# Kernel optimization log

Measured on AMD Instinct MI355X. Metric: run time of the kernel, lower is better.

## Reference

```python
import jax, jax.numpy as jnp
import numpy as np

H, O, M, D, B = 4, 32, 128, 16, 1024
JITTER = 1e-4


def k_rbf(theta, X, Y):
    # theta: [H, 1+D] (log sf2, log lengthscales); X: [O,Mx,D]; Y: [O,My,D]
    sf2 = jnp.exp(theta[:, 0])[:, None, None, None]          # [H,1,1,1]
    ls = jnp.exp(theta[:, 1:])                               # [H,D]
    Xs = X[None] / ls[:, None, None, :]                      # [H,O,Mx,D]
    Ys = Y[None] / ls[:, None, None, :]                      # [H,O,My,D]
    d2 = ((Xs ** 2).sum(-1)[..., :, None]
          + (Ys ** 2).sum(-1)[..., None, :]
          - 2.0 * jnp.einsum('homd,hond->homn', Xs, Ys))
    return sf2 * jnp.exp(-0.5 * jnp.maximum(d2, 0.0))


def vec2tril(vec, m):
    r, c = jnp.tril_indices(m)
    L = jnp.zeros(vec.shape[:-1] + (m, m), vec.dtype)
    return L.at[..., r, c].set(vec)


def _st(Lmat, rhs):
    return jax.scipy.linalg.solve_triangular(Lmat, rhs, lower=True)


def setup_inputs() -> dict:
    key = jax.random.key(0)
    ks = jax.random.split(key, 8)
    eye = jnp.eye(M, dtype=jnp.float32)
    return {
        'x': jax.random.normal(ks[0], (B, D), jnp.float32),
        'z': 0.5 * jax.random.normal(ks[1], (O, M, D), jnp.float32),
        'u_mean': 0.5 * jax.random.normal(ks[2], (O, M, 1), jnp.float32),
        'u_tril_vec': 0.1 * jax.random.normal(ks[3], (O, M * (M + 1) // 2), jnp.float32),
        'm_old': 0.5 * jax.random.normal(ks[4], (O, M, 1), jnp.float32),
        'L_old': jnp.tril(0.1 * jax.random.normal(ks[5], (O, M, M), jnp.float32)) + eye,
        'z_old': 0.5 * jax.random.normal(ks[6], (O, M, D), jnp.float32),
        'theta': 0.1 * jax.random.normal(ks[7], (H, D + 1), jnp.float32),
    }


def reference(x, z, u_mean, u_tril_vec, m_old, L_old, z_old, theta):
    dt = x.dtype
    u_tril = vec2tril(u_tril_vec, M)                          # [O,M,M]
    eyeM = jnp.eye(M, dtype=dt)

    # ---- linear_gauss_joint (one previous task) ----
    kuf = k_rbf(theta, z_old, z)                              # [H,O,M,M]
    kuu = k_rbf(theta, z_old, z_old)                          # [H,O,M,M]
    Lkuu = jnp.linalg.cholesky(kuu + JITTER * eyeM)
    LKinvKuf = _st(Lkuu, kuf)
    m_oldh = jnp.broadcast_to(m_old[None], (H, O, M, 1))
    L_oldh = jnp.broadcast_to(L_old[None], (H, O, M, M))
    LKinvm = _st(Lkuu, m_oldh)
    Am = jnp.einsum('...ij,...ik->...jk', LKinvKuf, LKinvm)   # A @ m_old, [H,O,M,1]
    m_new = Am + u_mean[None]
    m_joint = jnp.concatenate([m_oldh, m_new], axis=-2)       # [H,O,2M,1]

    S_old = jnp.einsum('...ji,...ki->...jk', L_oldh, L_oldh)
    LKinvLS = _st(Lkuu, L_oldh)
    AtX = jnp.einsum('...ij,...ik->...jk', LKinvLS, LKinvKuf)  # [H,O,M,M]
    SoldAt = jnp.einsum('...ji,...ik->...jk', L_oldh, AtX)
    ASoldt = jnp.swapaxes(SoldAt, -1, -2)
    S_cur = jnp.einsum('...ji,...ki->...jk', u_tril, u_tril)[None]
    ASoldAt = jnp.einsum('...ij,...ik->...jk', AtX, AtX)
    cov_joint = jnp.concatenate([
        jnp.concatenate([S_old, SoldAt], axis=-1),
        jnp.concatenate([ASoldt, S_cur + ASoldAt], axis=-1)], axis=-2)
    eye2M = jnp.eye(2 * M, dtype=dt)
    L_joint = jnp.linalg.cholesky(cov_joint + JITTER * eye2M)  # [H,O,2M,2M]
    z_joint = jnp.concatenate([z_old, z], axis=-2)             # [O,2M,D]

    # ---- linear_gauss_conditional_diag ----
    xb = jnp.broadcast_to(x[None], (O, B, D))
    kuf2 = k_rbf(theta, z_joint, xb)                           # [H,O,2M,B]
    kuu2 = k_rbf(theta, z_joint, z_joint)
    Lk2 = jnp.linalg.cholesky(kuu2 + JITTER * eye2M)
    LKinvu = _st(Lk2, m_joint)
    LKinvKuf2 = _st(Lk2, kuf2)
    kff_diag = jnp.exp(theta[:, 0])[:, None, None]             # [H,1,1]
    diag1 = (LKinvKuf2 ** 2).sum(axis=-2)                      # [H,O,B]
    LKinvLs = _st(Lk2, L_joint)
    vec2 = jnp.einsum('...ij,...ik->...jk', LKinvLs, LKinvKuf2)
    diag2 = (vec2 ** 2).sum(axis=-2)
    mu = jnp.einsum('...ij,...ik->...jk', LKinvKuf2, LKinvu)[..., 0]
    var = kff_diag - diag1 + diag2
    return mu, var
```

## Files before the change

### kernel.cpp

```cpp
#include <hip/hip_runtime.h>

#define H_ 4
#define O_ 32
#define HO 128
#define M_ 128
#define M2 256
#define D_ 16
#define B_ 1024
#define JIT 1e-4f

typedef unsigned short ushort_t;
typedef __bf16 v8bf __attribute__((ext_vector_type(8)));
typedef float v16f __attribute__((ext_vector_type(16)));
typedef unsigned short v8us __attribute__((ext_vector_type(8)));
typedef unsigned short v4us __attribute__((ext_vector_type(4)));

__device__ inline void splitbf(float v, ushort_t& hb, ushort_t& lb) {
    unsigned int u = __float_as_uint(v);
    hb = (ushort_t)(u >> 16);
    float hf = __uint_as_float((unsigned int)hb << 16);
    float r = v - hf;
    lb = (ushort_t)(__float_as_uint(r) >> 16);
}
__device__ inline float bf2f(ushort_t u) { return __uint_as_float((unsigned int)u << 16); }

__device__ __forceinline__ float rdlane(float v, int l) {
    return __int_as_float(__builtin_amdgcn_readlane(__float_as_int(v), l));
}

__global__ __launch_bounds__(256) void k_prekuu2(const float* __restrict__ theta,
                                                 const float* __restrict__ x,
                                                 const float* __restrict__ z,
                                                 const float* __restrict__ z_old,
                                                 float* __restrict__ SF2,
                                                 float* __restrict__ XS, float* __restrict__ XN,
                                                 float* __restrict__ ZS, float* __restrict__ ZN,
                                                 float* __restrict__ K2) {
    int bb = blockIdx.x, t = threadIdx.x;
    __shared__ float zs[M2][D_];
    __shared__ float zn[M2];
    __shared__ float ls[D_];
    if (bb == 144) {
        if (t < H_) SF2[t] = __expf(theta[t * (D_ + 1)]);
        return;
    }
    if (bb >= 128) {
        int j = (bb - 128) * 256 + t;
        int h = j >> 10, b = j & 1023;
        if (t < D_) ls[t] = __expf(-theta[h * (D_ + 1) + 1 + t]);
        __syncthreads();
        float s = 0.f;
#pragma unroll
        for (int d = 0; d < D_; d++) {
            float v = x[b * D_ + d] * ls[d];
            XS[(long)j * D_ + d] = v;
            s += v * v;
        }
        XN[j] = s;
        return;
    }
    int pair = bb, h = pair >> 5, o = pair & 31, i = t;
    if (t < D_) ls[t] = __expf(-theta[h * (D_ + 1) + 1 + t]);
    __syncthreads();
    const float* src = (i < M_) ? (z_old + ((long)o * M_ + i) * D_)
                                : (z + ((long)o * M_ + (i - M_)) * D_);
    float s = 0.f;
#pragma unroll
    for (int d = 0; d < D_; d++) {
        float v = src[d] * ls[d];
        zs[i][d] = v;
        ZS[((long)pair * M2 + i) * D_ + d] = v;
        s += v * v;
    }
    zn[i] = s;
    ZN[pair * M2 + i] = s;
    __syncthreads();
    float sf2 = __expf(theta[h * (D_ + 1)]);
    float my[D_];
#pragma unroll
    for (int d = 0; d < D_; d++) my[d] = zs[i][d];
    float myn = zn[i];
    for (int q = 0; q < M2; q++) {
        float dot = 0.f;
#pragma unroll
        for (int d = 0; d < D_; d++) dot += zs[q][d] * my[d];
        float d2 = fmaxf(zn[q] + myn - 2.f * dot, 0.f);
        float v = sf2 * __expf(-0.5f * d2);
        if (q == i) v += JIT;
        K2[(long)pair * M2 * M2 + (long)q * M2 + i] = v;
    }
}

__device__ __forceinline__ void choltri_body(const float* __restrict__ S, int ldsrc,
                                             float* __restrict__ Li, long b1, int t,
                                             float* __restrict__ Ap, float* __restrict__ Lv,
                                             float* __restrict__ Ws4, float* __restrict__ Tm) {
    for (int e = t; e < M_ * (M_ + 1) / 2; e += 256) {
        int i = (int)((sqrtf(8.f * e + 1.f) - 1.f) * 0.5f);
        while ((i + 1) * (i + 2) / 2 <= e) i++;
        while (i * (i + 1) / 2 > e) i--;
        int j = e - i * (i + 1) / 2;
        Ap[e] = S[(long)i * ldsrc + j];
    }
    __syncthreads();

    int lane = t & 63;
    int wav = t >> 6;
    int r = lane & 31;

    for (int kb = 0; kb < 4; kb++) {
        int c0 = kb * 32;
        if (wav == 0) {
            float a[32];
            int gr = c0 + r;
            int base = gr * (gr + 1) / 2 + c0;
#pragma unroll
            for (int j = 0; j < 32; j++) a[j] = Ap[base + j];
#pragma unroll
            for (int k = 0; k < 32; k++) {
                float dk = rdlane(a[k], k);
                float rs = rsqrtf(dk);
                rs = rs * (1.5f - 0.5f * dk * rs * rs);
                a[k] *= rs;
#pragma unroll
                for (int j = k + 1; j < 32; j++) {
                    float ljk = rdlane(a[k], j);
                    a[j] = fmaf(-a[k], ljk, a[j]);
                }
            }
            float wr[32];
#pragma unroll
            for (int i = 0; i < 32; i++) {
                float di = rdlane(a[i], i);
                float rdi = 1.0f / di;
                float acc = 0.f;
#pragma unroll
                for (int j = 0; j < i; j++) {
                    float lij = rdlane(a[j], i);
                    acc = fmaf(lij, wr[j], acc);
                }
                wr[i] = (i == r) ? rdi : -acc * rdi;
            }
            if (lane < 32) {
                float* Wp = Ws4 + kb * 1056;
#pragma unroll
                for (int i = 0; i < 32; i++) Wp[i * 33 + r] = wr[i];
            }
        }
        __syncthreads();
        int R = 96 - c0;
        if (R > 0) {
            if (t < R) {
                int gi = c0 + 32 + t;
                int pb = gi * (gi + 1) / 2 + c0;
                float xr[32];
#pragma unroll
                for (int j = 0; j < 32; j++) xr[j] = Ap[pb + j];
                const float* Wp = Ws4 + kb * 1056;
                float xo[32];
#pragma unroll
                for (int k = 0; k < 32; k++) {
                    float acc = 0.f;
#pragma unroll
                    for (int j = 0; j <= k; j++) acc = fmaf(xr[j], Wp[k * 33 + j], acc);
                    xo[k] = acc;
                }
#pragma unroll
                for (int k = 0; k < 32; k++) Ap[pb + k] = xo[k];
            }
            __syncthreads();
            int nb = R >> 2;
            int ntile = nb * (nb + 1) / 2;
            for (int tp = t; tp < ntile; tp += 256) {
                int bi = (int)((sqrtf(8.f * tp + 1.f) - 1.f) * 0.5f);
                while ((bi + 1) * (bi + 2) / 2 <= tp) bi++;
                while (bi * (bi + 1) / 2 > tp) bi--;
                int bj = tp - bi * (bi + 1) / 2;
                int i0 = c0 + 32 + bi * 4, j0 = c0 + 32 + bj * 4;
                float acc[4][4] = {};
                for (int k = 0; k < 32; k++) {
                    float av[4], bv[4];
#pragma unroll
                    for (int q = 0; q < 4; q++) av[q] = Ap[(i0 + q) * (i0 + q + 1) / 2 + c0 + k];
#pragma unroll
                    for (int rr = 0; rr < 4; rr++) bv[rr] = Ap[(j0 + rr) * (j0 + rr + 1) / 2 + c0 + k];
#pragma unroll
                    for (int q = 0; q < 4; q++)
#pragma unroll
                        for (int rr = 0; rr < 4; rr++) acc[q][rr] += av[q] * bv[rr];
                }
#pragma unroll
                for (int q = 0; q < 4; q++)
#pragma unroll
                    for (int rr = 0; rr < 4; rr++) {
                        int gi = i0 + q, gj = j0 + rr;
                        if (gj <= gi) Ap[gi * (gi + 1) / 2 + gj] -= acc[q][rr];
                    }
            }
            __syncthreads();
        }
    }

    for (int e = t; e < 16384; e += 256) {
        int i = e >> 7, j = e & 127;
        int bi = i >> 5, bj = j >> 5;
        float v = 0.f;
        if (bi == bj) v = Ws4[bi * 1056 + (i & 31) * 33 + (j & 31)];
        Lv[i * 132 + j] = v;
    }
    __syncthreads();
    for (int d = 1; d < 4; d++) {
        int nblk = 4 - d;
        int ne = nblk * 256;
        for (int p = t; p < ne; p += 256) {
            int b = p >> 8, rc = p & 255;
            int rr = rc >> 3, c4 = (rc & 7) * 4;
            int ib = b + d;
            int grow = ib * 32 + rr;
            int abase = grow * (grow + 1) / 2;
            float a0 = 0.f, a1 = 0.f, a2 = 0.f, a3 = 0.f;
            for (int k = b; k < ib; k++) {
                const float* Arow = Ap + abase + k * 32;
                const float* L0 = Lv + (k * 32) * 132 + b * 32 + c4;
#pragma unroll
                for (int q = 0; q < 32; q++) {
                    float av = Arow[q];
                    const float* Lr = L0 + q * 132;
                    a0 = fmaf(av, Lr[0], a0);
                    a1 = fmaf(av, Lr[1], a1);
                    a2 = fmaf(av, Lr[2], a2);
                    a3 = fmaf(av, Lr[3], a3);
                }
            }
            float* Tp = Tm + b * 1152 + rr * 36 + c4;
            Tp[0] = a0; Tp[1] = a1; Tp[2] = a2; Tp[3] = a3;
        }
        __syncthreads();
        for (int p = t; p < ne; p += 256) {
            int b = p >> 8, rc = p & 255;
            int rr = rc >> 3, c4 = (rc & 7) * 4;
            int ib = b + d;
            const float* Wp = Ws4 + ib * 1056 + rr * 33;
            const float* T0 = Tm + b * 1152 + c4;
            float a0 = 0.f, a1 = 0.f, a2 = 0.f, a3 = 0.f;
#pragma unroll
            for (int q = 0; q < 32; q++) {
                float wq = Wp[q];
                const float* Tq = T0 + q * 36;
                a0 = fmaf(wq, Tq[0], a0);
                a1 = fmaf(wq, Tq[1], a1);
                a2 = fmaf(wq, Tq[2], a2);
                a3 = fmaf(wq, Tq[3], a3);
            }
            float* Op = Lv + (ib * 32 + rr) * 132 + b * 32 + c4;
            Op[0] = -a0; Op[1] = -a1; Op[2] = -a2; Op[3] = -a3;
        }
        __syncthreads();
    }
    for (int e = t; e < 16384; e += 256) {
        int i = e >> 7, j = e & 127;
        Li[b1 + e] = Lv[i * 132 + j];
    }
}

#define SH_TOTAL (8256 + 16896 + 4224 + 3456)

__global__ __launch_bounds__(256) void k_choltri_tl(const float* __restrict__ src,
                                                    float* __restrict__ Li,
                                                    const float* __restrict__ L_old,
                                                    const float* __restrict__ vec,
                                                    ushort_t* __restrict__ WTh,
                                                    ushort_t* __restrict__ WTl) {
    int bb = blockIdx.x, t = threadIdx.x;
    __shared__ __align__(16) float SH[SH_TOTAL];
    if (bb < 128) {
        choltri_body(src + (long)bb * ((long)M2 * M2), M2, Li, (long)bb * 16384, t,
                     SH, SH + 8256, SH + 8256 + 16896, SH + 8256 + 16896 + 4224);
        return;
    }
    int pair = bb - 128, o = pair & 31;
    long b2 = (long)pair * 65536;
    float* vs = SH;
    float(*tile)[33] = (float(*)[33])(SH + 8256);
    for (int e = t; e < M_ * (M_ + 1) / 2; e += 256) vs[e] = vec[(long)o * (M_ * (M_ + 1) / 2) + e];
    __syncthreads();
    for (int e = t; e < 16384; e += 256) {
        int n = e >> 7, k = e & 127;
        float v = (k >= n) ? vs[k * (k + 1) / 2 + n] : 0.f;
        ushort_t hb, lb;
        splitbf(v, hb, lb);
        long a = b2 + (long)(128 + n) * 256 + 128 + k;
        WTh[a] = hb;
        WTl[a] = lb;
    }
    for (int e = t; e < 16384; e += 256) {
        int n = e >> 7, k = e & 127;
        long a = b2 + (long)(128 + n) * 256 + k;
        WTh[a] = 0;
        WTl[a] = 0;
    }
    const float* sp = L_old + (long)o * 16384;
    int tx = t & 31, ty = t >> 5;
    for (int bi = 0; bi < 4; bi++)
        for (int bj = 0; bj < 4; bj++) {
            __syncthreads();
            for (int r = ty; r < 32; r += 8)
                tile[r][tx] = sp[(long)(bi * 32 + r) * 128 + bj * 32 + tx];
            __syncthreads();
            for (int r = ty; r < 32; r += 8) {
                ushort_t hb, lb;
                splitbf(tile[tx][r], hb, lb);
                long a = b2 + (long)(bj * 32 + r) * 256 + bi * 32 + tx;
                WTh[a] = hb;
                WTl[a] = lb;
            }
        }
}

__global__ __launch_bounds__(256) void k_choltri_br(const float* __restrict__ src,
                                                    float* __restrict__ Li,
                                                    const float* __restrict__ A1,
                                                    const float* __restrict__ Linv1,
                                                    float* __restrict__ T1g,
                                                    const float* __restrict__ BLW,
                                                    ushort_t* __restrict__ LTh,
                                                    ushort_t* __restrict__ LTl,
                                                    ushort_t* __restrict__ WTh,
                                                    ushort_t* __restrict__ WTl) {
    int bb = blockIdx.x, t = threadIdx.x;
    __shared__ __align__(16) float SH[SH_TOTAL];
    if (bb < 128) {
        choltri_body(src + (long)bb * ((long)M2 * M2), M2, Li, (long)bb * 16384, t,
                     SH, SH + 8256, SH + 8256 + 16896, SH + 8256 + 16896 + 4224);
        return;
    }
    if (bb < 256) {
        int pair = bb - 128;
        long b1 = (long)pair * 16384;
        float(*As)[132] = (float(*)[132])(SH + 8256);
        float(*Bs)[132] = ((float(*)[132])(SH + 8256)) + 16;
        const float* Apt = A1 + b1;
        const float* Bpt = Linv1 + b1;
        float* Cp = T1g + (long)pair * 65536;
        int tx = t & 15, ty = t >> 4;
        float acc[8][8] = {};
        for (int kt = 0; kt < M_; kt += 16) {
#pragma unroll
            for (int q = 0; q < 8; q++) {
                int e = q * 256 + t;
                int kk = e >> 7, m = e & 127;
                As[kk][m] = Apt[(long)(kt + kk) * 128 + m];
                Bs[kk][m] = Bpt[(long)(kt + kk) * 128 + m];
            }
            __syncthreads();
#pragma unroll
            for (int kk = 0; kk < 16; kk++) {
                float a[8], b[8];
#pragma unroll
                for (int q = 0; q < 8; q++) { a[q] = As[kk][ty + 16 * q]; b[q] = Bs[kk][tx + 16 * q]; }
#pragma unroll
                for (int q = 0; q < 8; q++)
#pragma unroll
                    for (int r = 0; r < 8; r++) acc[q][r] += a[q] * b[r];
            }
            __syncthreads();
        }
#pragma unroll
        for (int q = 0; q < 8; q++)
#pragma unroll
            for (int r = 0; r < 8; r++)
                Cp[(long)(ty + 16 * q) * 128 + tx + 16 * r] = acc[q][r];
        return;
    }
    if (bb < 384) {
        int pair = bb - 256;
        long b2 = (long)pair * 65536, b1 = (long)pair * 16384;
        float(*tile)[33] = (float(*)[33])(SH + 8256);
        for (int e = t; e < 16384; e += 256) {
            int n = e >> 7, k = e & 127;
            long a = b2 + (long)(128 + n) * 256 + k;
            LTh[a] = 0;
            LTl[a] = 0;
        }
        const float* sp = Linv1 + b1;
        int tx = t & 31, ty = t >> 5;
        for (int bi = 0; bi < 4; bi++)
            for (int bj = 0; bj < 4; bj++) {
                __syncthreads();
                for (int r = ty; r < 32; r += 8)
                    tile[r][tx] = sp[(long)(bi * 32 + r) * 128 + bj * 32 + tx];
                __syncthreads();
                for (int r = ty; r < 32; r += 8) {
                    ushort_t hb, lb;
                    splitbf(tile[tx][r], hb, lb);
                    long a = b2 + (long)(bj * 32 + r) * 256 + bi * 32 + tx;
                    LTh[a] = hb;
                    LTl[a] = lb;
                }
            }
        return;
    }
    {
        int pair = bb - 384;
        long b2 = (long)pair * 65536, b1 = (long)pair * 16384;
        float(*tile)[33] = (float(*)[33])(SH + 8256);
        const float* sp = BLW + b1;
        int tx = t & 31, ty = t >> 5;
        for (int bi = 0; bi < 4; bi++)
            for (int bj = 0; bj < 4; bj++) {
                __syncthreads();
                for (int r = ty; r < 32; r += 8)
                    tile[r][tx] = sp[(long)(bi * 32 + r) * 128 + bj * 32 + tx];
                __syncthreads();
                for (int r = ty; r < 32; r += 8) {
                    ushort_t hb, lb;
                    splitbf(tile[tx][r], hb, lb);
                    long a = b2 + (long)(bj * 32 + r) * 256 + 128 + bi * 32 + tx;
                    WTh[a] = hb;
                    WTl[a] = lb;
                }
            }
    }
}

__global__ __launch_bounds__(256) void k_a1a3(const float* __restrict__ Linv1,
                                              const float* __restrict__ KUU2,
                                              const float* __restrict__ L_old,
                                              float* __restrict__ A1, float* __restrict__ A3) {
    int pair = blockIdx.x, y = blockIdx.y, o = pair & 31;
    const float* Ap = Linv1 + (long)pair * 16384;
    const float* Bp = y ? (L_old + (long)o * 16384) : (KUU2 + (long)pair * 65536 + 128);
    int ldb = y ? 128 : 256;
    float* Cp = (y ? A3 : A1) + (long)pair * 16384;
    int t = threadIdx.x, tx = t & 15, ty = t >> 4;
    __shared__ float As[16][132], Bs[16][132];
    float acc[8][8] = {};
    for (int kt = 0; kt < M_; kt += 16) {
#pragma unroll
        for (int q = 0; q < 8; q++) {
            int e = q * 256 + t;
            int m = e >> 4, kk = e & 15;
            As[kk][m] = Ap[(long)m * 128 + kt + kk];
            int kk2 = e >> 7, n = e & 127;
            Bs[kk2][n] = Bp[(long)(kt + kk2) * ldb + n];
        }
        __syncthreads();
#pragma unroll
        for (int kk = 0; kk < 16; kk++) {
            float a[8], b[8];
#pragma unroll
            for (int q = 0; q < 8; q++) { a[q] = As[kk][ty + 16 * q]; b[q] = Bs[kk][tx + 16 * q]; }
#pragma unroll
            for (int q = 0; q < 8; q++)
#pragma unroll
                for (int r = 0; r < 8; r++) acc[q][r] += a[q] * b[r];
        }
        __syncthreads();
    }
#pragma unroll
    for (int q = 0; q < 8; q++)
#pragma unroll
        for (int r = 0; r < 8; r++)
            Cp[(long)(ty + 16 * q) * 128 + tx + 16 * r] = acc[q][r];
}

__global__ __launch_bounds__(256) void k_blwschur(const float* __restrict__ A1,
                                                  const float* __restrict__ A3,
                                                  float* __restrict__ BLW,
                                                  float* __restrict__ KUU2,
                                                  const float* __restrict__ Linv1,
                                                  const float* __restrict__ m_old,
                                                  const float* __restrict__ u_mean,
                                                  float* __restrict__ MJ,
                                                  float* __restrict__ CV) {
    int pair = blockIdx.x, y = blockIdx.y, o = pair & 31;
    int t = threadIdx.x;
    if (y == 2) {
        CV[pair * 256 + t] = 0.f;
        __shared__ float mo[128], a2[128];
        if (t < 128) mo[t] = m_old[o * 128 + t];
        __syncthreads();
        if (t < 128) {
            const float* Lr = Linv1 + (long)pair * 16384 + (long)t * 128;
            float acc = 0.f;
            for (int j = 0; j <= t; j++) acc += Lr[j] * mo[j];
            a2[t] = acc;
        }
        __syncthreads();
        if (t < 128) {
            float m = 0.f;
            for (int i = 0; i < 128; i++) m += A1[(long)pair * 16384 + (long)i * 128 + t] * a2[i];
            MJ[pair * 256 + t] = mo[t];
            MJ[pair * 256 + 128 + t] = m + u_mean[o * 128 + t];
        }
        return;
    }
    const float* Ap = A1 + (long)pair * 16384;
    const float* Bp = (y ? A1 : A3) + (long)pair * 16384;
    float* Cp;
    int ldc;
    if (y) { Cp = KUU2 + (long)pair * 65536 + 128L * 256 + 128; ldc = 256; }
    else   { Cp = BLW + (long)pair * 16384; ldc = 128; }
    int tx = t & 15, ty = t >> 4;
    __shared__ float As[16][132], Bs[16][132];
    float acc[8][8] = {};
    for (int kt = 0; kt < M_; kt += 16) {
#pragma unroll
        for (int q = 0; q < 8; q++) {
            int e = q * 256 + t;
            int kk = e >> 7, m = e & 127;
            As[kk][m] = Ap[(long)(kt + kk) * 128 + m];
            Bs[kk][m] = Bp[(long)(kt + kk) * 128 + m];
        }
        __syncthreads();
#pragma unroll
        for (int kk = 0; kk < 16; kk++) {
            float a[8], b[8];
#pragma unroll
            for (int q = 0; q < 8; q++) { a[q] = As[kk][ty + 16 * q]; b[q] = Bs[kk][tx + 16 * q]; }
#pragma unroll
            for (int q = 0; q < 8; q++)
#pragma unroll
                for (int r = 0; r < 8; r++) acc[q][r] += a[q] * b[r];
        }
        __syncthreads();
    }
#pragma unroll
    for (int q = 0; q < 8; q++)
#pragma unroll
        for (int r = 0; r < 8; r++) {
            long idx = (long)(ty + 16 * q) * ldc + tx + 16 * r;
            if (y) Cp[idx] -= acc[q][r];
            else Cp[idx] = acc[q][r];
        }
}

__global__ __launch_bounds__(256) void k_blicalc2(const float* __restrict__ Linv2,
                                                  const float* __restrict__ T1g,
                                                  ushort_t* __restrict__ LTh,
                                                  ushort_t* __restrict__ LTl) {
    int pair = blockIdx.x, t = threadIdx.x, tx = t & 15, ty = t >> 4;
    long b1 = (long)pair * 16384, b2 = (long)pair * 65536;
    __shared__ float T1s[128][129];
    __shared__ float As[16][132], Bs[16][132];
    const float* Apt = Linv2 + b1;
    const float* Bpt = T1g + (long)pair * 65536;
    float acc[8][8] = {};
    for (int kt = 0; kt < M_; kt += 16) {
#pragma unroll
        for (int q = 0; q < 8; q++) {
            int e = q * 256 + t;
            int m = e >> 4, kk = e & 15;
            As[kk][m] = Apt[(long)m * 128 + kt + kk];
            int kk2 = e >> 7, n = e & 127;
            Bs[kk2][n] = Bpt[(long)(kt + kk2) * 128 + n];
        }
        __syncthreads();
#pragma unroll
        for (int kk = 0; kk < 16; kk++) {
            float a[8], b[8];
#pragma unroll
            for (int q = 0; q < 8; q++) { a[q] = As[kk][ty + 16 * q]; b[q] = Bs[kk][tx + 16 * q]; }
#pragma unroll
            for (int q = 0; q < 8; q++)
#pragma unroll
                for (int r = 0; r < 8; r++) acc[q][r] += a[q] * b[r];
        }
        __syncthreads();
    }
#pragma unroll
    for (int q = 0; q < 8; q++)
#pragma unroll
        for (int r = 0; r < 8; r++) T1s[ty + 16 * q][tx + 16 * r] = -acc[q][r];
    __syncthreads();
    for (int e = t; e < 16384; e += 256) {
        int j = e >> 7, i = e & 127;
        ushort_t hb, lb;
        splitbf(T1s[i][j], hb, lb);
        long a = b2 + (long)j * 256 + 128 + i;
        LTh[a] = hb;
        LTl[a] = lb;
    }
    __syncthreads();
    for (int e = t; e < 16384; e += 256) {
        int i = e >> 7, j = e & 127;
        T1s[i][j] = Apt[(long)i * 128 + j];
    }
    __syncthreads();
    for (int e = t; e < 16384; e += 256) {
        int n = e >> 7, k = e & 127;
        ushort_t hb, lb;
        splitbf(T1s[k][n], hb, lb);
        long a = b2 + (long)(128 + n) * 256 + 128 + k;
        LTh[a] = hb;
        LTl[a] = lb;
    }
}

#define BSTR 56
template <int TILES3>
__global__ __launch_bounds__(256) void k_bmmx(const ushort_t* __restrict__ Ah,
                                              const ushort_t* __restrict__ Al,
                                              const ushort_t* __restrict__ Bh,
                                              const ushort_t* __restrict__ Bl,
                                              float* __restrict__ Cf,
                                              ushort_t* __restrict__ Chi,
                                              ushort_t* __restrict__ Clo,
                                              const float* __restrict__ Dm,
                                              int kLoMode, float alpha,
                                              const float* __restrict__ MJv,
                                              float* __restrict__ CVat) {
    int pair = blockIdx.x;
    long base = (long)pair * 65536;
    int I0, J0, mir = 0;
    if (TILES3) {
        int qb = blockIdx.y;
        I0 = (qb == 0) ? 0 : 128;
        J0 = (qb == 2) ? 0 : I0;
        mir = (qb == 2);
    } else {
        I0 = (blockIdx.y >> 1) * 128;
        J0 = (blockIdx.y & 1) * 128;
    }
    int k0 = (kLoMode == 1) ? max(I0, J0) : (kLoMode == 2) ? J0 : 0;
    int t = threadIdx.x;
    int w = t >> 6, lane = t & 63;
    int l31 = lane & 31, lhalf = lane >> 5;
    int wy = w >> 1, wx = w & 1;

    __shared__ __align__(16) ushort_t AsH[128][BSTR], AsL[128][BSTR];
    __shared__ __align__(16) ushort_t BsH[128][BSTR], BsL[128][BSTR];

    v16f acc[2][2];
#pragma unroll
    for (int mt = 0; mt < 2; mt++)
#pragma unroll
        for (int nt = 0; nt < 2; nt++)
#pragma unroll
            for (int r = 0; r < 16; r++) acc[mt][nt][r] = 0.f;

    for (int kt = k0; kt < 256; kt += 32) {
        __syncthreads();
#pragma unroll
        for (int u = 0; u < 2; u++) {
            int idx = u * 256 + t;
            int m = idx >> 2, kc = (idx & 3) * 8;
            long arow = base + (long)(I0 + m) * 256 + kt + kc;
            long brow = base + (long)(J0 + m) * 256 + kt + kc;
            *(v8us*)&AsH[m][kc] = *(const v8us*)(Ah + arow);
            *(v8us*)&AsL[m][kc] = *(const v8us*)(Al + arow);
            *(v8us*)&BsH[m][kc] = *(const v8us*)(Bh + brow);
            *(v8us*)&BsL[m][kc] = *(const v8us*)(Bl + brow);
        }
        __syncthreads();
#pragma unroll
        for (int ks = 0; ks < 2; ks++) {
            int ko = ks * 16 + lhalf * 8;
            v8bf ah[2], al[2], bh[2], bl[2];
#pragma unroll
            for (int mt = 0; mt < 2; mt++) {
                int r = wy * 64 + mt * 32 + l31;
                ah[mt] = *(const v8bf*)&AsH[r][ko];
                al[mt] = *(const v8bf*)&AsL[r][ko];
            }
#pragma unroll
            for (int nt = 0; nt < 2; nt++) {
                int r = wx * 64 + nt * 32 + l31;
                bh[nt] = *(const v8bf*)&BsH[r][ko];
                bl[nt] = *(const v8bf*)&BsL[r][ko];
            }
#pragma unroll
            for (int mt = 0; mt < 2; mt++)
#pragma unroll
                for (int nt = 0; nt < 2; nt++) {
                    acc[mt][nt] = __builtin_amdgcn_mfma_f32_32x32x16_bf16(ah[mt], bh[nt], acc[mt][nt], 0, 0, 0);
                    acc[mt][nt] = __builtin_amdgcn_mfma_f32_32x32x16_bf16(ah[mt], bl[nt], acc[mt][nt], 0, 0, 0);
                    acc[mt][nt] = __builtin_amdgcn_mfma_f32_32x32x16_bf16(al[mt], bh[nt], acc[mt][nt], 0, 0, 0);
                }
        }
    }

    float mjc[2] = {0.f, 0.f};
    float cvmir[2] = {0.f, 0.f};
    if (MJv) {
#pragma unroll
        for (int nt = 0; nt < 2; nt++)
            mjc[nt] = MJv[(long)pair * 256 + J0 + wx * 64 + nt * 32 + l31];
    }
#pragma unroll
    for (int mt = 0; mt < 2; mt++) {
#pragma unroll
        for (int r = 0; r < 16; r++) {
            int row = I0 + wy * 64 + mt * 32 + 8 * (r >> 2) + 4 * lhalf + (r & 3);
            float rowsum = 0.f;
            float mjrow = 0.f;
            if (MJv && mir) mjrow = MJv[(long)pair * 256 + row];
#pragma unroll
            for (int nt = 0; nt < 2; nt++) {
                int col = J0 + wx * 64 + nt * 32 + l31;
                long idx = base + (long)row * 256 + col;
                float v = alpha * acc[mt][nt][r];
                if (Dm) v += Dm[idx];
                ushort_t hb, lb;
                splitbf(v, hb, lb);
                if (Cf) Cf[idx] = v;
                if (Chi) { Chi[idx] = hb; Clo[idx] = lb; }
                if (mir) {
                    long idxT = base + (long)col * 256 + row;
                    if (Cf) Cf[idxT] = v;
                    if (Chi) { Chi[idxT] = hb; Clo[idxT] = lb; }
                }
                if (MJv) {
                    rowsum += v * mjc[nt];
                    if (mir) cvmir[nt] += v * mjrow;
                }
            }
            if (MJv) {
#pragma unroll
                for (int m = 1; m < 32; m <<= 1) rowsum += __shfl_xor(rowsum, m, 64);
                if (l31 == 0) atomicAdd(&CVat[(long)pair * 256 + row], rowsum);
            }
        }
    }
    if (MJv && mir) {
#pragma unroll
        for (int nt = 0; nt < 2; nt++)
            atomicAdd(&CVat[(long)pair * 256 + J0 + wx * 64 + nt * 32 + l31], cvmir[nt]);
    }
}

#define KTP 280
__global__ __launch_bounds__(256) void k_kbuild(const float* __restrict__ ZS, const float* __restrict__ ZN,
                                                const float* __restrict__ XS, const float* __restrict__ XN,
                                                const float* __restrict__ SF2, const float* __restrict__ CV,
                                                ushort_t* __restrict__ Kg, float* __restrict__ out) {
    int bt = blockIdx.x;
    int pair = blockIdx.y;
    int h = pair >> 5;
    int t = threadIdx.x;
    int w = t >> 6;
    int b = t & 63;

    __shared__ __align__(16) ushort_t KbT[64][KTP];
    __shared__ float mup[4][64];

    float sf2 = SF2[h];
    long bg = (long)h * B_ + bt * 64 + b;
    const float4* xrow = (const float4*)(XS + bg * 16);
    float4 x0 = xrow[0], x1 = xrow[1], x2 = xrow[2], x3 = xrow[3];
    float xn = XN[bg];
    float mupart = 0.f;
    const float* cvp = CV + pair * 256;
    const float* znp = ZN + pair * 256;
#pragma unroll 2
    for (int j8 = 0; j8 < 8; j8++) {
        v8us kb8;
#pragma unroll
        for (int e = 0; e < 8; e++) {
            int j = w * 64 + j8 * 8 + e;
            const float4* zrow = (const float4*)(ZS + ((long)pair * 256 + j) * 16);
            float4 z0 = zrow[0], z1 = zrow[1], z2 = zrow[2], z3 = zrow[3];
            float dot = z0.x * x0.x + z0.y * x0.y + z0.z * x0.z + z0.w * x0.w +
                        z1.x * x1.x + z1.y * x1.y + z1.z * x1.z + z1.w * x1.w +
                        z2.x * x2.x + z2.y * x2.y + z2.z * x2.z + z2.w * x2.w +
                        z3.x * x3.x + z3.y * x3.y + z3.z * x3.z + z3.w * x3.w;
            float d2 = fmaxf(znp[j] + xn - 2.f * dot, 0.f);
            float kv = sf2 * __expf(-0.5f * d2);
            mupart += cvp[j] * kv;
            unsigned int u = __float_as_uint(kv);
            u += 0x7fffu + ((u >> 16) & 1u);
            kb8[e] = (unsigned short)(u >> 16);
        }
        *(v8us*)&KbT[b][w * 64 + j8 * 8] = kb8;
    }
    mup[w][b] = mupart;
    __syncthreads();
    long kbase = ((long)pair * 1024 + bt * 64) * 256;
#pragma unroll
    for (int e = 0; e < 8; e++) {
        int c = e * 256 + t;
        int bb = c >> 5, cj = (c & 31) * 8;
        *(v8us*)(Kg + kbase + (long)bb * 256 + cj) = *(const v8us*)&KbT[bb][cj];
    }
    if (t < 64) {
        float mu = mup[0][t] + mup[1][t] + mup[2][t] + mup[3][t];
        out[(long)pair * 1024 + bt * 64 + t] = mu;
    }
}

#define KT2 264
__global__ __launch_bounds__(256) void k_kb4(const ushort_t* __restrict__ Kg,
                                             const ushort_t* __restrict__ Ghi,
                                             const ushort_t* __restrict__ Glo,
                                             const float* __restrict__ SF2, float* __restrict__ out) {
    int pair = blockIdx.x & 127;
    int bt = blockIdx.x >> 7;
    int h = pair >> 5;
    int t = threadIdx.x;
    int w = t >> 6;
    int lane = t & 63;
    int l31 = lane & 31, lhalf = lane >> 5;

    __shared__ __align__(16) ushort_t KbT[128][KT2];
    __shared__ float qpart[4][128];

    float sf2 = SF2[h];
    long kbase = ((long)pair * 1024 + bt * 128) * 256;
#pragma unroll
    for (int e = 0; e < 16; e++) {
        int c = e * 256 + t;
        int bb = c >> 5, cj = (c & 31) * 8;
        *(v8us*)&KbT[bb][cj] = *(const v8us*)(Kg + kbase + (long)bb * 256 + cj);
    }
    __syncthreads();

    v16f acc[2][4];
#pragma unroll
    for (int mt = 0; mt < 2; mt++)
#pragma unroll
        for (int nt = 0; nt < 4; nt++)
#pragma unroll
            for (int r = 0; r < 16; r++) acc[mt][nt][r] = 0.f;

    const ushort_t* GhiP = Ghi + (long)pair * 65536;
    const ushort_t* GloP = Glo + (long)pair * 65536;
#pragma unroll 2
    for (int k0 = 0; k0 < 256; k0 += 16) {
        v8bf bfr[4];
#pragma unroll
        for (int nt = 0; nt < 4; nt++)
            bfr[nt] = *(const v8bf*)&KbT[nt * 32 + l31][k0 + lhalf * 8];
#pragma unroll
        for (int mt = 0; mt < 2; mt++) {
            int i = w * 64 + mt * 32 + l31;
            v8bf ah = *(const v8bf*)(GhiP + (long)i * 256 + k0 + lhalf * 8);
            v8bf al = *(const v8bf*)(GloP + (long)i * 256 + k0 + lhalf * 8);
#pragma unroll
            for (int nt = 0; nt < 4; nt++) {
                acc[mt][nt] = __builtin_amdgcn_mfma_f32_32x32x16_bf16(ah, bfr[nt], acc[mt][nt], 0, 0, 0);
                acc[mt][nt] = __builtin_amdgcn_mfma_f32_32x32x16_bf16(al, bfr[nt], acc[mt][nt], 0, 0, 0);
            }
        }
    }

    float qp[4] = {0.f, 0.f, 0.f, 0.f};
#pragma unroll
    for (int mt = 0; mt < 2; mt++) {
#pragma unroll
        for (int nt = 0; nt < 4; nt++) {
            int b = nt * 32 + l31;
#pragma unroll
            for (int g = 0; g < 4; g++) {
                int ibase = w * 64 + mt * 32 + 8 * g + 4 * lhalf;
                v4us k4 = *(const v4us*)&KbT[b][ibase];
#pragma unroll
                for (int e = 0; e < 4; e++) {
                    float kv = bf2f(k4[e]);
                    qp[nt] += kv * acc[mt][nt][4 * g + e];
                }
            }
        }
    }
#pragma unroll
    for (int nt = 0; nt < 4; nt++) {
        qp[nt] += __shfl_down(qp[nt], 32, 64);
        if (lhalf == 0) qpart[w][nt * 32 + l31] = qp[nt];
    }
    __syncthreads();

    if (t < 128) {
        float q = qpart[0][t] + qpart[1][t] + qpart[2][t] + qpart[3][t];
        out[(long)H_ * O_ * B_ + (long)pair * 1024 + bt * 128 + t] = sf2 - q;
    }
}

extern "C" void kernel_launch(void* const* d_in, const int* in_sizes, int n_in,
                              void* d_out, int out_size, void* d_ws, size_t ws_size,
                              hipStream_t stream) {
    const float* x = (const float*)d_in[0];
    const float* z = (const float*)d_in[1];
    const float* u_mean = (const float*)d_in[2];
    const float* u_tril_vec = (const float*)d_in[3];
    const float* m_old = (const float*)d_in[4];
    const float* L_old = (const float*)d_in[5];
    const float* z_old = (const float*)d_in[6];
    const float* theta = (const float*)d_in[7];

    const long BIGSZ = (long)HO * M2 * M2;
    const long MSZ = (long)HO * M_ * M_;

    float* ws = (float*)d_ws;
    long off = 0;
    float* BIG0 = ws + off; off += BIGSZ;
    float* BIG1 = ws + off; off += BIGSZ;
    float* BIG2 = ws + off; off += BIGSZ;
    float* BIG3 = ws + off; off += BIGSZ;
    float* ZS = ws + off; off += (long)HO * M2 * D_;
    float* XS = ws + off; off += (long)H_ * B_ * D_;
    float* ZN = ws + off; off += (long)HO * M2;
    float* XN = ws + off; off += (long)H_ * B_;
    float* MJ = ws + off; off += (long)HO * M2;
    float* CV = ws + off; off += (long)HO * M2;
    float* SF2v = ws + off; off += H_;

    float* KUU2 = BIG0;
    float* AINV = BIG0;
    float* T1g = BIG0;
    float* Linv1 = BIG2;
    float* A1 = BIG2 + MSZ;
    float* A3 = BIG2 + 2 * MSZ;
    float* Linv2 = BIG2 + 2 * MSZ;
    float* BLW = BIG2 + 3 * MSZ;
    ushort_t* LINVTh = (ushort_t*)BIG1;
    ushort_t* LINVTl = LINVTh + BIGSZ;
    ushort_t* AINVh = (ushort_t*)BIG2;
    ushort_t* AINVl = AINVh + BIGSZ;
    ushort_t* WcTh = (ushort_t*)BIG3;
    ushort_t* WcTl = WcTh + BIGSZ;
    ushort_t* Yh = (ushort_t*)BIG1;
    ushort_t* Yl = Yh + BIGSZ;
    ushort_t* Ghi = (ushort_t*)BIG3;
    ushort_t* Glo = Ghi + BIGSZ;
    ushort_t* Kg = (ushort_t*)BIG1;
    const long BRoff = 128L * M2 + 128;

    k_prekuu2<<<145, 256, 0, stream>>>(theta, x, z, z_old, SF2v, XS, XN, ZS, ZN, KUU2);
    k_choltri_tl<<<256, 256, 0, stream>>>(KUU2, Linv1, L_old, u_tril_vec, WcTh, WcTl);
    k_a1a3<<<dim3(HO, 2), 256, 0, stream>>>(Linv1, KUU2, L_old, A1, A3);
    k_blwschur<<<dim3(HO, 3), 256, 0, stream>>>(A1, A3, BLW, KUU2, Linv1, m_old, u_mean, MJ, CV);
    k_choltri_br<<<512, 256, 0, stream>>>(KUU2 + BRoff, Linv2, A1, Linv1, T1g, BLW,
                                          LINVTh, LINVTl, WcTh, WcTl);
    k_blicalc2<<<HO, 256, 0, stream>>>(Linv2, T1g, LINVTh, LINVTl);
    k_bmmx<1><<<dim3(HO, 3), 256, 0, stream>>>(LINVTh, LINVTl, LINVTh, LINVTl,
                                               AINV, AINVh, AINVl, nullptr, 1, 1.f, MJ, CV);
    k_bmmx<0><<<dim3(HO, 4), 256, 0, stream>>>(AINVh, AINVl, WcTh, WcTl,
                                               nullptr, Yh, Yl, nullptr, 2, 1.f, nullptr, nullptr);
    k_bmmx<1><<<dim3(HO, 3), 256, 0, stream>>>(Yh, Yl, Yh, Yl,
                                               nullptr, Ghi, Glo, AINV, 0, -1.f, nullptr, nullptr);
    k_kbuild<<<dim3(16, HO), 256, 0, stream>>>(ZS, ZN, XS, XN, SF2v, CV, Kg, (float*)d_out);
    k_kb4<<<1024, 256, 0, stream>>>(Kg, Ghi, Glo, SF2v, (float*)d_out);
}
```

Baseline: 624.5 us.

## Restructure Cholesky-inverse kernels: 512 threads, smaller LDS, deferred diag-block inversion

Doubles the block size of the two Cholesky/triangular-inverse kernels to 512 threads and cuts LDS use by dropping the padded Lv staging buffer. Intermediate inverse blocks are now written straight to global memory and read back with float4 loads. The panel solve now does forward substitution with stored reciprocal diagonals instead of multiplying by an explicit 32x32 inverse. All four diagonal-block inversions are computed in parallel by four waves after the factorization, rather than serially inside each panel step. This aims to raise occupancy and parallelism, at the cost of extra global traffic and a zero-fill of the output.

New measurement: 746.8 us. 19.6% more time.

```diff
diff --git a/kernel.cpp b/kernel.cpp
--- a/kernel.cpp
+++ b/kernel.cpp
@@ -93,14 +93,26 @@
 
 __device__ __forceinline__ void choltri_body(const float* __restrict__ S, int ldsrc,
                                              float* __restrict__ Li, long b1, int t,
-                                             float* __restrict__ Ap, float* __restrict__ Lv,
-                                             float* __restrict__ Ws4, float* __restrict__ Tm) {
-    for (int e = t; e < M_ * (M_ + 1) / 2; e += 256) {
-        int i = (int)((sqrtf(8.f * e + 1.f) - 1.f) * 0.5f);
-        while ((i + 1) * (i + 2) / 2 <= e) i++;
-        while (i * (i + 1) / 2 > e) i--;
-        int j = e - i * (i + 1) / 2;
-        Ap[e] = S[(long)i * ldsrc + j];
+                                             float* __restrict__ Ap, float* __restrict__ Ws4,
+                                             float* __restrict__ Tm, float* __restrict__ rdia) {
+    {
+        float4 z4 = make_float4(0.f, 0.f, 0.f, 0.f);
+#pragma unroll
+        for (int u = 0; u < 8; u++) {
+            int e = u * 512 + t;
+            *(float4*)(Li + b1 + (long)e * 4) = z4;
+        }
+    }
+#pragma unroll
+    for (int u = 0; u < 8; u++) {
+        int idx = u * 512 + t;
+        int i = idx >> 5, jc = (idx & 31) * 4;
+        float4 v = *(const float4*)(S + (long)i * ldsrc + jc);
+        int tb = i * (i + 1) / 2 + jc;
+        if (jc + 0 <= i) Ap[tb + 0] = v.x;
+        if (jc + 1 <= i) Ap[tb + 1] = v.y;
+        if (jc + 2 <= i) Ap[tb + 2] = v.z;
+        if (jc + 3 <= i) Ap[tb + 3] = v.w;
     }
     __syncthreads();
 
@@ -122,29 +134,17 @@
                 float rs = rsqrtf(dk);
                 rs = rs * (1.5f - 0.5f * dk * rs * rs);
                 a[k] *= rs;
+                if (lane == k) rdia[c0 + k] = rs;
 #pragma unroll
                 for (int j = k + 1; j < 32; j++) {
                     float ljk = rdlane(a[k], j);
                     a[j] = fmaf(-a[k], ljk, a[j]);
                 }
             }
-            float wr[32];
-#pragma unroll
-            for (int i = 0; i < 32; i++) {
-                float di = rdlane(a[i], i);
-                float rdi = 1.0f / di;
-                float acc = 0.f;
-#pragma unroll
-                for (int j = 0; j < i; j++) {
-                    float lij = rdlane(a[j], i);
-                    acc = fmaf(lij, wr[j], acc);
-                }
-                wr[i] = (i == r) ? rdi : -acc * rdi;
-            }
             if (lane < 32) {
-                float* Wp = Ws4 + kb * 1056;
-#pragma unroll
-                for (int i = 0; i < 32; i++) Wp[i * 33 + r] = wr[i];
+#pragma unroll
+                for (int j = 0; j < 32; j++)
+                    if (j <= r) Ap[base + j] = a[j];
             }
         }
         __syncthreads();
@@ -156,22 +156,21 @@
                 float xr[32];
 #pragma unroll
                 for (int j = 0; j < 32; j++) xr[j] = Ap[pb + j];
-                const float* Wp = Ws4 + kb * 1056;
-                float xo[32];
-#pragma unroll
-                for (int k = 0; k < 32; k++) {
-                    float acc = 0.f;
-#pragma unroll
-                    for (int j = 0; j <= k; j++) acc = fmaf(xr[j], Wp[k * 33 + j], acc);
-                    xo[k] = acc;
+#pragma unroll
+                for (int q = 0; q < 32; q++) {
+                    float xq = xr[q] * rdia[c0 + q];
+                    xr[q] = xq;
+#pragma unroll
+                    for (int j = q + 1; j < 32; j++)
+                        xr[j] = fmaf(-xq, Ap[(c0 + j) * (c0 + j + 1) / 2 + c0 + q], xr[j]);
                 }
 #pragma unroll
-                for (int k = 0; k < 32; k++) Ap[pb + k] = xo[k];
+                for (int j = 0; j < 32; j++) Ap[pb + j] = xr[j];
             }
             __syncthreads();
             int nb = R >> 2;
             int ntile = nb * (nb + 1) / 2;
-            for (int tp = t; tp < ntile; tp += 256) {
+            for (int tp = t; tp < ntile; tp += 512) {
                 int bi = (int)((sqrtf(8.f * tp + 1.f) - 1.f) * 0.5f);
                 while ((bi + 1) * (bi + 2) / 2 <= tp) bi++;
                 while (bi * (bi + 1) / 2 > tp) bi--;
@@ -201,18 +200,44 @@
         }
     }
 
-    for (int e = t; e < 16384; e += 256) {
-        int i = e >> 7, j = e & 127;
-        int bi = i >> 5, bj = j >> 5;
-        float v = 0.f;
-        if (bi == bj) v = Ws4[bi * 1056 + (i & 31) * 33 + (j & 31)];
-        Lv[i * 132 + j] = v;
-    }
-    __syncthreads();
+    if (wav < 4) {
+        int pb = wav;
+        int c0 = pb * 32;
+        float a[32];
+        int gr = c0 + r;
+        int base = gr * (gr + 1) / 2 + c0;
+#pragma unroll
+        for (int j = 0; j < 32; j++) a[j] = Ap[base + j];
+        float wr[32];
+#pragma unroll
+        for (int i = 0; i < 32; i++) {
+            float rdi = rdia[c0 + i];
+            float acc = 0.f;
+#pragma unroll
+            for (int j = 0; j < i; j++) {
+                float lij = rdlane(a[j], i);
+                acc = fmaf(lij, wr[j], acc);
+            }
+            wr[i] = (i == r) ? rdi : -acc * rdi;
+        }
+        if (lane < 32) {
+            float* Wp = Ws4 + pb * 1056;
+#pragma unroll
+            for (int i = 0; i < 32; i++) Wp[i * 33 + r] = wr[i];
+        }
+    }
+    __syncthreads();
+
+    for (int e = t; e < 4096; e += 512) {
+        int g = e >> 10, rr2 = (e >> 5) & 31, cc = e & 31;
+        Li[b1 + (long)(g * 32 + rr2) * 128 + g * 32 + cc] = Ws4[g * 1056 + rr2 * 33 + cc];
+    }
+    __syncthreads();
+
     for (int d = 1; d < 4; d++) {
         int nblk = 4 - d;
         int ne = nblk * 256;
-        for (int p = t; p < ne; p += 256) {
+        for (int p = t; p < ne; p += 512) {
             int b = p >> 8, rc = p & 255;
             int rr = rc >> 3, c4 = (rc & 7) * 4;
             int ib = b + d;
@@ -221,22 +246,22 @@
             float a0 = 0.f, a1 = 0.f, a2 = 0.f, a3 = 0.f;
             for (int k = b; k < ib; k++) {
                 const float* Arow = Ap + abase + k * 32;
-                const float* L0 = Lv + (k * 32) * 132 + b * 32 + c4;
+                const float* Lg = Li + b1 + (long)(k * 32) * 128 + b * 32 + c4;
 #pragma unroll
                 for (int q = 0; q < 32; q++) {
                     float av = Arow[q];
-                    const float* Lr = L0 + q * 132;
-                    a0 = fmaf(av, Lr[0], a0);
-                    a1 = fmaf(av, Lr[1], a1);
-                    a2 = fmaf(av, Lr[2], a2);
-                    a3 = fmaf(av, Lr[3], a3);
+                    float4 lv = *(const float4*)(Lg + (long)q * 128);
+                    a0 = fmaf(av, lv.x, a0);
+                    a1 = fmaf(av, lv.y, a1);
+                    a2 = fmaf(av, lv.z, a2);
+                    a3 = fmaf(av, lv.w, a3);
                 }
             }
             float* Tp = Tm + b * 1152 + rr * 36 + c4;
             Tp[0] = a0; Tp[1] = a1; Tp[2] = a2; Tp[3] = a3;
         }
         __syncthreads();
-        for (int p = t; p < ne; p += 256) {
+        for (int p = t; p < ne; p += 512) {
             int b = p >> 8, rc = p & 255;
             int rr = rc >> 3, c4 = (rc & 7) * 4;
             int ib = b + d;
@@ -252,39 +277,35 @@
                 a2 = fmaf(wq, Tq[2], a2);
                 a3 = fmaf(wq, Tq[3], a3);
             }
-            float* Op = Lv + (ib * 32 + rr) * 132 + b * 32 + c4;
-            Op[0] = -a0; Op[1] = -a1; Op[2] = -a2; Op[3] = -a3;
-        }
-        __syncthreads();
-    }
-    for (int e = t; e < 16384; e += 256) {
-        int i = e >> 7, j = e & 127;
-        Li[b1 + e] = Lv[i * 132 + j];
-    }
-}
-
-#define SH_TOTAL (8256 + 16896 + 4224 + 3456)
-
-__global__ __launch_bounds__(256) void k_choltri_tl(const float* __restrict__ src,
-                                                    float* __restrict__ Li,
-                                                    const float* __restrict__ L_old,
-                                                    const float* __restrict__ vec,
-                                                    ushort_t* __restrict__ WTh,
-                                                    ushort_t* __restrict__ WTl) {
+            *(float4*)(Li + b1 + (long)(ib * 32 + rr) * 128 + b * 32 + c4) =
+                make_float4(-a0, -a1, -a2, -a3);
+        }
+        __syncthreads();
+    }
+}
+
+#define SH_TOTAL (8256 + 4224 + 3456 + 128)
+
+__global__ __launch_bounds__(512, 2) void k_choltri_tl(const float* __restrict__ src,
+                                                       float* __restrict__ Li,
+                                                       const float* __restrict__ L_old,
+                                                       const float* __restrict__ vec,
+                                                       ushort_t* __restrict__ WTh,
+                                                       ushort_t* __restrict__ WTl) {
     int bb = blockIdx.x, t = threadIdx.x;
     __shared__ __align__(16) float SH[SH_TOTAL];
     if (bb < 128) {
         choltri_body(src + (long)bb * ((long)M2 * M2), M2, Li, (long)bb * 16384, t,
-                     SH, SH + 8256, SH + 8256 + 16896, SH + 8256 + 16896 + 4224);
+                     SH, SH + 8256, SH + 8256 + 4224, SH + 8256 + 4224 + 3456);
         return;
     }
     int pair = bb - 128, o = pair & 31;
     long b2 = (long)pair * 65536;
     float* vs = SH;
     float(*tile)[33] = (float(*)[33])(SH + 8256);
-    for (int e = t; e < M_ * (M_ + 1) / 2; e += 256) vs[e] = vec[(long)o * (M_ * (M_ + 1) / 2) + e];
-    __syncthreads();
-    for (int e = t; e < 16384; e += 256) {
+    for (int e = t; e < M_ * (M_ + 1) / 2; e += 512) vs[e] = vec[(long)o * (M_ * (M_ + 1) / 2) + e];
+    __syncthreads();
+    for (int e = t; e < 16384; e += 512) {
         int n = e >> 7, k = e & 127;
         float v = (k >= n) ? vs[k * (k + 1) / 2 + n] : 0.f;
         ushort_t hb, lb;
@@ -293,7 +314,7 @@
         WTh[a] = hb;
         WTl[a] = lb;
     }
-    for (int e = t; e < 16384; e += 256) {
+    for (int e = t; e < 16384; e += 512) {
         int n = e >> 7, k = e & 127;
         long a = b2 + (long)(128 + n) * 256 + k;
         WTh[a] = 0;
@@ -304,10 +325,10 @@
     for (int bi = 0; bi < 4; bi++)
         for (int bj = 0; bj < 4; bj++) {
             __syncthreads();
-            for (int r = ty; r < 32; r += 8)
+            for (int r = ty; r < 32; r += 16)
                 tile[r][tx] = sp[(long)(bi * 32 + r) * 128 + bj * 32 + tx];
             __syncthreads();
-            for (int r = ty; r < 32; r += 8) {
+            for (int r = ty; r < 32; r += 16) {
                 ushort_t hb, lb;
                 splitbf(tile[tx][r], hb, lb);
                 long a = b2 + (long)(bj * 32 + r) * 256 + bi * 32 + tx;
@@ -317,21 +338,21 @@
         }
 }
 
-__global__ __launch_bounds__(256) void k_choltri_br(const float* __restrict__ src,
-                                                    float* __restrict__ Li,
-                                                    const float* __restrict__ A1,
-                                                    const float* __restrict__ Linv1,
-                                                    float* __restrict__ T1g,
-                                                    const float* __restrict__ BLW,
-                                                    ushort_t* __restrict__ LTh,
-                                                    ushort_t* __restrict__ LTl,
-                                                    ushort_t* __restrict__ WTh,
-                                                    ushort_t* __restrict__ WTl) {
+__global__ __launch_bounds__(512, 2) void k_choltri_br(const float* __restrict__ src,
+                                                       float* __restrict__ Li,
+                                                       const float* __restrict__ A1,
+                                                       const float* __restrict__ Linv1,
+                                                       float* __restrict__ T1g,
+                                                       const float* __restrict__ BLW,
+                                                       ushort_t* __restrict__ LTh,
+                                                       ushort_t* __restrict__ LTl,
+                                                       ushort_t* __restrict__ WTh,
+                                                       ushort_t* __restrict__ WTl) {
     int bb = blockIdx.x, t = threadIdx.x;
     __shared__ __align__(16) float SH[SH_TOTAL];
     if (bb < 128) {
         choltri_body(src + (long)bb * ((long)M2 * M2), M2, Li, (long)bb * 16384, t,
-                     SH, SH + 8256, SH + 8256 + 16896, SH + 8256 + 16896 + 4224);
+                     SH, SH + 8256, SH + 8256 + 4224, SH + 8256 + 4224 + 3456);
         return;
     }
     if (bb < 256) {
@@ -343,11 +364,11 @@
         const float* Bpt = Linv1 + b1;
         float* Cp = T1g + (long)pair * 65536;
         int tx = t & 15, ty = t >> 4;
-        float acc[8][8] = {};
+        float acc[4][8] = {};
         for (int kt = 0; kt < M_; kt += 16) {
 #pragma unroll
-            for (int q = 0; q < 8; q++) {
-                int e = q * 256 + t;
+            for (int q = 0; q < 4; q++) {
+                int e = q * 512 + t;
                 int kk = e >> 7, m = e & 127;
                 As[kk][m] = Apt[(long)(kt + kk) * 128 + m];
                 Bs[kk][m] = Bpt[(long)(kt + kk) * 128 + m];
@@ -355,28 +376,30 @@
             __syncthreads();
 #pragma unroll
             for (int kk = 0; kk < 16; kk++) {
-                float a[8], b[8];
-#pragma unroll
-                for (int q = 0; q < 8; q++) { a[q] = As[kk][ty + 16 * q]; b[q] = Bs[kk][tx + 16 * q]; }
-#pragma unroll
-                for (int q = 0; q < 8; q++)
+                float a[4], b[8];
+#pragma unroll
+                for (int q = 0; q < 4; q++) a[q] = As[kk][ty + 32 * q];
+#pragma unroll
+                for (int r = 0; r < 8; r++) b[r] = Bs[kk][tx + 16 * r];
+#pragma unroll
+                for (int q = 0; q < 4; q++)
 #pragma unroll
                     for (int r = 0; r < 8; r++) acc[q][r] += a[q] * b[r];
             }
             __syncthreads();
         }
 #pragma unroll
-        for (int q = 0; q < 8; q++)
+        for (int q = 0; q < 4; q++)
 #pragma unroll
             for (int r = 0; r < 8; r++)
-                Cp[(long)(ty + 16 * q) * 128 + tx + 16 * r] = acc[q][r];
+                Cp[(long)(ty + 32 * q) * 128 + tx + 16 * r] = acc[q][r];
         return;
     }
     if (bb < 384) {
         int pair = bb - 256;
         long b2 = (long)pair * 65536, b1 = (long)pair * 16384;
         float(*tile)[33] = (float(*)[33])(SH + 8256);
-        for (int e = t; e < 16384; e += 256) {
+        for (int e = t; e < 16384; e += 512) {
             int n = e >> 7, k = e & 127;
             long a = b2 + (long)(128 + n) * 256 + k;
             LTh[a] = 0;
@@ -387,10 +410,10 @@
         for (int bi = 0; bi < 4; bi++)
             for (int bj = 0; bj < 4; bj++) {
                 __syncthreads();
-                for (int r = ty; r < 32; r += 8)
+                for (int r = ty; r < 32; r += 16)
                     tile[r][tx] = sp[(long)(bi * 32 + r) * 128 + bj * 32 + tx];
                 __syncthreads();
-                for (int r = ty; r < 32; r += 8) {
+                for (int r = ty; r < 32; r += 16) {
                     ushort_t hb, lb;
                     splitbf(tile[tx][r], hb, lb);
                     long a = b2 + (long)(bj * 32 + r) * 256 + bi * 32 + tx;
@@ -409,10 +432,10 @@
         for (int bi = 0; bi < 4; bi++)
             for (int bj = 0; bj < 4; bj++) {
                 __syncthreads();
-                for (int r = ty; r < 32; r += 8)
+                for (int r = ty; r < 32; r += 16)
                     tile[r][tx] = sp[(long)(bi * 32 + r) * 128 + bj * 32 + tx];
                 __syncthreads();
-                for (int r = ty; r < 32; r += 8) {
+                for (int r = ty; r < 32; r += 16) {
                     ushort_t hb, lb;
                     splitbf(tile[tx][r], hb, lb);
                     long a = b2 + (long)(bj * 32 + r) * 256 + 128 + bi * 32 + tx;
@@ -925,10 +948,10 @@
     const long BRoff = 128L * M2 + 128;
 
     k_prekuu2<<<145, 256, 0, stream>>>(theta, x, z, z_old, SF2v, XS, XN, ZS, ZN, KUU2);
-    k_choltri_tl<<<256, 256, 0, stream>>>(KUU2, Linv1, L_old, u_tril_vec, WcTh, WcTl);
+    k_choltri_tl<<<256, 512, 0, stream>>>(KUU2, Linv1, L_old, u_tril_vec, WcTh, WcTl);
     k_a1a3<<<dim3(HO, 2), 256, 0, stream>>>(Linv1, KUU2, L_old, A1, A3);
     k_blwschur<<<dim3(HO, 3), 256, 0, stream>>>(A1, A3, BLW, KUU2, Linv1, m_old, u_mean, MJ, CV);
-    k_choltri_br<<<512, 256, 0, stream>>>(KUU2 + BRoff, Linv2, A1, Linv1, T1g, BLW,
+    k_choltri_br<<<512, 512, 0, stream>>>(KUU2 + BRoff, Linv2, A1, Linv1, T1g, BLW,
                                           LINVTh, LINVTl, WcTh, WcTl);
     k_blicalc2<<<HO, 256, 0, stream>>>(Linv2, T1g, LINVTh, LINVTl);
     k_bmmx<1><<<dim3(HO, 3), 256, 0, stream>>>(LINVTh, LINVTl, LINVTh, LINVTl,
```

## Defer diagonal-block inversions to end and parallelize across four waves

Applied to the files above, without the earlier changes.

The blocked Cholesky previously had wave 0 invert each 32x32 diagonal block serially inside the panel loop, then applied that inverse to the panel rows. Now the panel update uses a forward substitution with stored reciprocal diagonals, reading the factor directly from the packed shared array. The four diagonal-block inversions move to after the factorization, where each of the four waves handles one block at the same time. This shortens the serial critical path per panel step, at the cost of more shared-memory reads in the triangular solve and a small extra shared buffer.

Result: faster. 611.2 us (-2.1%).

```diff
diff --git a/kernel.cpp b/kernel.cpp
--- a/kernel.cpp
+++ b/kernel.cpp
@@ -94,7 +94,8 @@
 __device__ __forceinline__ void choltri_body(const float* __restrict__ S, int ldsrc,
                                              float* __restrict__ Li, long b1, int t,
                                              float* __restrict__ Ap, float* __restrict__ Lv,
-                                             float* __restrict__ Ws4, float* __restrict__ Tm) {
+                                             float* __restrict__ Ws4, float* __restrict__ Tm,
+                                             float* __restrict__ rdia) {
     for (int e = t; e < M_ * (M_ + 1) / 2; e += 256) {
         int i = (int)((sqrtf(8.f * e + 1.f) - 1.f) * 0.5f);
         while ((i + 1) * (i + 2) / 2 <= e) i++;
@@ -122,29 +123,17 @@
                 float rs = rsqrtf(dk);
                 rs = rs * (1.5f - 0.5f * dk * rs * rs);
                 a[k] *= rs;
+                if (lane == k) rdia[c0 + k] = rs;
 #pragma unroll
                 for (int j = k + 1; j < 32; j++) {
                     float ljk = rdlane(a[k], j);
                     a[j] = fmaf(-a[k], ljk, a[j]);
                 }
             }
-            float wr[32];
-#pragma unroll
-            for (int i = 0; i < 32; i++) {
-                float di = rdlane(a[i], i);
-                float rdi = 1.0f / di;
-                float acc = 0.f;
-#pragma unroll
-                for (int j = 0; j < i; j++) {
-                    float lij = rdlane(a[j], i);
-                    acc = fmaf(lij, wr[j], acc);
-                }
-                wr[i] = (i == r) ? rdi : -acc * rdi;
-            }
             if (lane < 32) {
-                float* Wp = Ws4 + kb * 1056;
-#pragma unroll
-                for (int i = 0; i < 32; i++) Wp[i * 33 + r] = wr[i];
+#pragma unroll
+                for (int j = 0; j < 32; j++)
+                    if (j <= r) Ap[base + j] = a[j];
             }
         }
         __syncthreads();
@@ -156,17 +145,16 @@
                 float xr[32];
 #pragma unroll
                 for (int j = 0; j < 32; j++) xr[j] = Ap[pb + j];
-                const float* Wp = Ws4 + kb * 1056;
-                float xo[32];
-#pragma unroll
-                for (int k = 0; k < 32; k++) {
-                    float acc = 0.f;
-#pragma unroll
-                    for (int j = 0; j <= k; j++) acc = fmaf(xr[j], Wp[k * 33 + j], acc);
-                    xo[k] = acc;
+#pragma unroll
+                for (int q = 0; q < 32; q++) {
+                    float xq = xr[q] * rdia[c0 + q];
+                    xr[q] = xq;
+#pragma unroll
+                    for (int j = q + 1; j < 32; j++)
+                        xr[j] = fmaf(-xq, Ap[(c0 + j) * (c0 + j + 1) / 2 + c0 + q], xr[j]);
                 }
 #pragma unroll
-                for (int k = 0; k < 32; k++) Ap[pb + k] = xo[k];
+                for (int j = 0; j < 32; j++) Ap[pb + j] = xr[j];
             }
             __syncthreads();
             int nb = R >> 2;
@@ -200,6 +188,34 @@
             __syncthreads();
         }
     }
+
+    {
+        int pb = wav;
+        int c0 = pb * 32;
+        float a[32];
+        int gr = c0 + r;
+        int base = gr * (gr + 1) / 2 + c0;
+#pragma unroll
+        for (int j = 0; j < 32; j++) a[j] = Ap[base + j];
+        float wr[32];
+#pragma unroll
+        for (int i = 0; i < 32; i++) {
+            float rdi = rdia[c0 + i];
+            float acc = 0.f;
+#pragma unroll
+            for (int j = 0; j < i; j++) {
+                float lij = rdlane(a[j], i);
+                acc = fmaf(lij, wr[j], acc);
+            }
+            wr[i] = (i == r) ? rdi : -acc * rdi;
+        }
+        if (lane < 32) {
+            float* Wp = Ws4 + pb * 1056;
+#pragma unroll
+            for (int i = 0; i < 32; i++) Wp[i * 33 + r] = wr[i];
+        }
+    }
+    __syncthreads();
 
     for (int e = t; e < 16384; e += 256) {
         int i = e >> 7, j = e & 127;
@@ -263,7 +279,7 @@
     }
 }
 
-#define SH_TOTAL (8256 + 16896 + 4224 + 3456)
+#define SH_TOTAL (8256 + 16896 + 4224 + 3456 + 128)
 
 __global__ __launch_bounds__(256) void k_choltri_tl(const float* __restrict__ src,
                                                     float* __restrict__ Li,
@@ -275,7 +291,8 @@
     __shared__ __align__(16) float SH[SH_TOTAL];
     if (bb < 128) {
         choltri_body(src + (long)bb * ((long)M2 * M2), M2, Li, (long)bb * 16384, t,
-                     SH, SH + 8256, SH + 8256 + 16896, SH + 8256 + 16896 + 4224);
+                     SH, SH + 8256, SH + 8256 + 16896, SH + 8256 + 16896 + 4224,
+                     SH + 8256 + 16896 + 4224 + 3456);
         return;
     }
     int pair = bb - 128, o = pair & 31;
@@ -331,7 +348,8 @@
     __shared__ __align__(16) float SH[SH_TOTAL];
     if (bb < 128) {
         choltri_body(src + (long)bb * ((long)M2 * M2), M2, Li, (long)bb * 16384, t,
-                     SH, SH + 8256, SH + 8256 + 16896, SH + 8256 + 16896 + 4224);
+                     SH, SH + 8256, SH + 8256 + 16896, SH + 8256 + 16896 + 4224,
+                     SH + 8256 + 16896 + 4224 + 3456);
         return;
     }
     if (bb < 256) {
```
